# Kernel optimization log

Measured on AMD Instinct MI355X. Metric: run time of the kernel, lower is better.

## Reference

```python
import jax, jax.numpy as jnp
import numpy as np

NUM_CLASSES = 2
THRESHOLD = 0.35
NEGPOS_RATIO = 7
VARIANCES = (0.1, 0.2)
B, P, O = 64, 16800, 64  # batch, num_priors, num_objs per image


def point_form(pr):
    # cxcywh -> xyxy
    return jnp.concatenate([pr[:, :2] - pr[:, 2:] / 2, pr[:, :2] + pr[:, 2:] / 2], axis=1)


def jaccard(a, b):
    # a: [A,4] xyxy, b: [Bx,4] xyxy -> IoU [A,Bx]
    lt = jnp.maximum(a[:, None, :2], b[None, :, :2])
    rb = jnp.minimum(a[:, None, 2:], b[None, :, 2:])
    wh = jnp.clip(rb - lt, 0.0)
    inter = wh[..., 0] * wh[..., 1]
    area_a = ((a[:, 2] - a[:, 0]) * (a[:, 3] - a[:, 1]))[:, None]
    area_b = ((b[:, 2] - b[:, 0]) * (b[:, 3] - b[:, 1]))[None, :]
    return inter / (area_a + area_b - inter)


def encode(matched, priors):
    # matched xyxy [P,4], priors cxcywh [P,4]
    g_cxcy = (matched[:, :2] + matched[:, 2:]) / 2 - priors[:, :2]
    g_cxcy = g_cxcy / (VARIANCES[0] * priors[:, 2:])
    g_wh = (matched[:, 2:] - matched[:, :2]) / priors[:, 2:]
    g_wh = jnp.log(g_wh) / VARIANCES[1]
    return jnp.concatenate([g_cxcy, g_wh], axis=1)


def encode_landm(matched, priors):
    # matched [P,10] -> [P,5,2]
    m = matched.reshape(-1, 5, 2)
    g = (m - priors[:, None, :2]) / (VARIANCES[0] * priors[:, None, 2:])
    return g.reshape(-1, 10)


def match_one(truths, labels, landms, priors):
    # truths [O,4], labels [O], landms [O,10]
    overlaps = jaccard(truths, point_form(priors))  # [O,P]
    best_prior_overlap = overlaps.max(axis=1)       # per-gt best IoU
    best_prior_idx = overlaps.argmax(axis=1)
    valid_gt = best_prior_overlap >= 0.2
    best_truth_overlap = overlaps.max(axis=0)       # per-prior best IoU
    best_truth_idx = overlaps.argmax(axis=0)
    # index_fill(2) only for valid gts (best_prior_idx_filter)
    bto = best_truth_overlap.at[best_prior_idx].set(
        jnp.where(valid_gt, 2.0, best_truth_overlap[best_prior_idx]))
    # ensure every gt keeps its best prior
    bti = best_truth_idx.at[best_prior_idx].set(jnp.arange(truths.shape[0]))
    matches = truths[bti]                  # [P,4]
    conf = labels[bti]                     # [P]
    conf = jnp.where(bto < THRESHOLD, 0.0, conf)
    loc = encode(matches, priors)
    landm = encode_landm(landms[bti], priors)
    return loc, conf, landm


def smooth_l1_sum(x, mask):
    ax = jnp.abs(x)
    v = jnp.where(ax < 1.0, 0.5 * ax * ax, ax - 0.5)
    return (v * mask).sum()


def setup_inputs() -> dict:
    key = jax.random.key(0)
    k1, k2, k3, k4, k5, k6, k7, k8 = jax.random.split(key, 8)
    loc_data = jax.random.normal(k1, (B, P, 4), jnp.float32)
    conf_data = jax.random.normal(k2, (B, P, NUM_CLASSES), jnp.float32)
    landm_data = jax.random.normal(k3, (B, P, 10), jnp.float32)
    # priors: cx,cy in (0,1), w,h in (0.02,0.22)
    cxy = jax.random.uniform(k4, (P, 2), jnp.float32)
    wh = jax.random.uniform(k5, (P, 2), jnp.float32) * 0.2 + 0.02
    priors = jnp.concatenate([cxy, wh], axis=1)
    # targets: valid corner boxes + landmarks + label in {1,-1}
    xy1 = jax.random.uniform(k6, (B, O, 2), jnp.float32) * 0.6
    bwh = jax.random.uniform(k7, (B, O, 2), jnp.float32) * 0.3 + 0.05
    boxes = jnp.concatenate([xy1, xy1 + bwh], axis=-1)
    lms = jax.random.uniform(k8, (B, O, 10), jnp.float32)
    lab = jnp.where(jax.random.uniform(jax.random.fold_in(key, 9), (B, O, 1)) < 0.3, -1.0, 1.0)
    targets = jnp.concatenate([boxes, lms, lab], axis=-1)
    return {"loc_data": loc_data, "conf_data": conf_data, "landm_data": landm_data,
            "priors": priors, "targets": targets}


def reference(loc_data, conf_data, landm_data, priors, targets):
    num = loc_data.shape[0]
    num_priors = priors.shape[0]
    truths = targets[:, :, :4]
    landms = targets[:, :, 4:14]
    labels = targets[:, :, -1]
    loc_t, conf_t, landm_t = jax.vmap(match_one, in_axes=(0, 0, 0, None))(
        truths, labels, landms, priors)  # [B,P,4], [B,P], [B,P,10]

    # landmark loss over conf_t > 0
    pos1 = conf_t > 0
    num_pos_landm = pos1.astype(jnp.int32).sum(axis=1, keepdims=True)
    N1 = jnp.maximum(num_pos_landm.sum().astype(jnp.float32), 1.0)
    loss_landm = smooth_l1_sum(landm_data - landm_t, pos1[..., None].astype(landm_data.dtype))

    # localization loss over conf_t != 0 ; conf_t[pos] = 1
    pos = conf_t != 0
    conf_t01 = jnp.where(pos, 1, 0)  # int {0,1}
    loss_l = smooth_l1_sum(loc_data - loc_t, pos[..., None].astype(loc_data.dtype))

    # hard negative mining on per-prior CE loss (global-max log_sum_exp, as in source)
    batch_conf = conf_data.reshape(-1, NUM_CLASSES)
    x_max = batch_conf.max()
    lse = jnp.log(jnp.exp(batch_conf - x_max).sum(axis=1, keepdims=True)) + x_max
    gathered = jnp.take_along_axis(batch_conf, conf_t01.reshape(-1, 1), axis=1)
    loss_c = (lse - gathered).reshape(num, -1)  # [B,P]; positives NOT zeroed (as in source)
    loss_idx = jnp.argsort(-loss_c, axis=1)
    idx_rank = jnp.argsort(loss_idx, axis=1)
    num_pos = pos.astype(jnp.int32).sum(axis=1, keepdims=True)  # [B,1]
    num_neg = jnp.minimum(NEGPOS_RATIO * num_pos, num_priors - 1)
    neg = idx_rank < num_neg  # [B,P]
    neg_pos = pos | neg

    # cross-entropy (sum) over selected pos+neg priors
    logp = jax.nn.log_softmax(conf_data, axis=-1)  # [B,P,C]
    ce = -jnp.take_along_axis(logp, conf_t01[..., None], axis=-1)[..., 0]
    loss_c_final = (ce * neg_pos.astype(ce.dtype)).sum()

    N = jnp.maximum(num_pos.sum().astype(jnp.float32), 1.0)
    return (loss_l / N, loss_c_final / N, loss_landm / N1)
```

## Files before the change

kernel.cpp:

```cpp
#include <hip/hip_runtime.h>
#include <math.h>

#define BN 64
#define PN 16800
#define ON 64
#define THRESH 0.35f
#define NEGPOS 7
#define GX 66
#define NBLK (BN * GX)
#define NBP 1024
#define NBTT (BN * GX)
#define NCELL 256
#define NCB 66
#define EPSW 0.0009765625f
#define IOUF 0.3499f
#define NBINS 4096
#define MAXM 4096
#define TAILT 104

struct GAcc {
  unsigned ticket;
  float sl, slm, sc;
  int np, np1;
  unsigned pad0, pad1;
};

__device__ __forceinline__ unsigned f2key(float f) {
  unsigned u = __float_as_uint(f);
  return (u & 0x80000000u) ? ~u : (u | 0x80000000u);
}
__device__ __forceinline__ float key2f(unsigned k) {
  unsigned u = (k & 0x80000000u) ? (k & 0x7FFFFFFFu) : ~k;
  return __uint_as_float(u);
}
__device__ __forceinline__ float sl1(float d) {
  float a = fabsf(d);
  return (a < 1.f) ? 0.5f * a * a : a - 0.5f;
}

__global__ void k_count(const float* __restrict__ priors,
                        unsigned char* __restrict__ pcell,
                        unsigned* __restrict__ gcnt,
                        unsigned* __restrict__ gmax) {
  __shared__ unsigned lcnt[NCELL];
  int tid = threadIdx.x;
  lcnt[tid] = 0;
  __syncthreads();
  int p = blockIdx.x * 256 + tid;
  float mw = 0.f, mh = 0.f;
  if (p < PN) {
    float4 pr = reinterpret_cast<const float4*>(priors)[p];
    int cx = (int)(pr.x * 16.f); cx = cx < 0 ? 0 : (cx > 15 ? 15 : cx);
    int cy = (int)(pr.y * 16.f); cy = cy < 0 ? 0 : (cy > 15 ? 15 : cy);
    int cell = cy * 16 + cx;
    pcell[p] = (unsigned char)cell;
    atomicAdd(&lcnt[cell], 1u);
    mw = pr.z * 0.5f;
    mh = pr.w * 0.5f;
  }
#pragma unroll
  for (int off = 32; off; off >>= 1) {
    mw = fmaxf(mw, __shfl_xor(mw, off));
    mh = fmaxf(mh, __shfl_xor(mh, off));
  }
  if ((tid & 63) == 0) {
    atomicMax(&gmax[0], __float_as_uint(mw));
    atomicMax(&gmax[1], __float_as_uint(mh));
  }
  __syncthreads();
  unsigned c = lcnt[tid];
  if (c) atomicAdd(&gcnt[tid], c);
}

__global__ void k_scatter(const float* __restrict__ priors,
                          const float* __restrict__ targets,
                          const unsigned char* __restrict__ pcell,
                          const unsigned* __restrict__ gcnt,
                          unsigned* __restrict__ gcur,
                          const unsigned* __restrict__ gmax,
                          float4* __restrict__ sbox,
                          int* __restrict__ sorig,
                          int* __restrict__ scell,
                          int* __restrict__ inv,
                          int* __restrict__ cellOff,
                          unsigned long long* __restrict__ tmask) {
  int bid = blockIdx.x;
  int tid = threadIdx.x;
  if (bid < NCB) {
    __shared__ unsigned tmp[NCELL];
    __shared__ unsigned excl[NCELL];
    __shared__ unsigned lcnt[NCELL];
    __shared__ unsigned lbase[NCELL];
    unsigned c = gcnt[tid];
    tmp[tid] = c;
    lcnt[tid] = 0;
    __syncthreads();
    for (int off = 1; off < NCELL; off <<= 1) {
      unsigned v = (tid >= off) ? tmp[tid - off] : 0u;
      __syncthreads();
      tmp[tid] += v;
      __syncthreads();
    }
    excl[tid] = tmp[tid] - c;
    if (bid == 0) {
      cellOff[tid] = (int)(tmp[tid] - c);
      if (tid == 0) cellOff[NCELL] = PN;
    }
    __syncthreads();
    int p = bid * 256 + tid;
    bool valid = p < PN;
    int cell = 0; unsigned lrank = 0;
    if (valid) {
      cell = pcell[p];
      lrank = atomicAdd(&lcnt[cell], 1u);
    }
    __syncthreads();
    if (lcnt[tid]) lbase[tid] = atomicAdd(&gcur[tid], lcnt[tid]);
    __syncthreads();
    if (valid) {
      int slot = (int)(excl[cell] + lbase[cell] + lrank);
      float4 pr = reinterpret_cast<const float4*>(priors)[p];
      float px1 = pr.x - pr.z * 0.5f, py1 = pr.y - pr.w * 0.5f;
      float px2 = pr.x + pr.z * 0.5f, py2 = pr.y + pr.w * 0.5f;
      sbox[slot] = make_float4(px1, py1, px2, py2);
      sorig[slot] = p;
      scell[slot] = cell;
      inv[p] = slot;
    }
  } else {
    int b = bid - NCB;
    __shared__ float4 tb[ON];
    if (tid < ON) {
      const float* tg = &targets[((long)b * ON + tid) * 15];
      tb[tid] = make_float4(tg[0], tg[1], tg[2], tg[3]);
    }
    __syncthreads();
    float MW = __uint_as_float(gmax[0]), MH = __uint_as_float(gmax[1]);
    int cx = tid & 15, cy = tid >> 4;
    float cxl = (float)cx * 0.0625f, cxh = (float)(cx + 1) * 0.0625f;
    float cyl = (float)cy * 0.0625f, cyh = (float)(cy + 1) * 0.0625f;
    float pmaxa = 4.f * MW * MH;
    unsigned long long m = 0ull;
    for (int t = 0; t < ON; t++) {
      float4 a = tb[t];
      float wt = a.z - a.x, ht = a.w - a.y;
      float at = wt * ht;
      float need = IOUF * at;
      float wmin = need / fminf(ht, 2.f * MH);
      float hmin = need / fminf(wt, 2.f * MW);
      float wx0 = a.x + wmin - MW - EPSW, wx1 = a.z - wmin + MW + EPSW;
      float wy0 = a.y + hmin - MH - EPSW, wy1 = a.w - hmin + MH + EPSW;
      bool ok = (pmaxa >= need) &&
                (cxh > wx0) && (cxl < wx1) &&
                (cyh > wy0) && (cyl < wy1);
      if (ok) m |= (1ull << t);
    }
    tmask[b * NCELL + tid] = m;
  }
}

__global__ void k_pair(const float* __restrict__ targets,
                       const float4* __restrict__ sbox,
                       const int* __restrict__ sorig,
                       const int* __restrict__ scell,
                       const int* __restrict__ cellOff,
                       const unsigned* __restrict__ gmax,
                       const unsigned long long* __restrict__ tmask,
                       unsigned char* __restrict__ btpack,
                       unsigned long long* __restrict__ bpp) {
  int bid = blockIdx.x;
  int tid = threadIdx.x;

  if (bid < NBP) {
    int lane = tid & 63, wv = tid >> 6;
    int b = bid >> 4;
    int t = ((bid & 15) << 2) + wv;
    const float* tg = &targets[((long)b * ON + t) * 15];
    float ax1 = tg[0], ay1 = tg[1], ax2 = tg[2], ay2 = tg[3];
    float aa = (ax2 - ax1) * (ay2 - ay1);
    float MW = __uint_as_float(gmax[0]), MH = __uint_as_float(gmax[1]);
    int xlo = (int)floorf((ax1 - MW - EPSW) * 16.f); xlo = xlo < 0 ? 0 : (xlo > 15 ? 15 : xlo);
    int xhi = (int)floorf((ax2 + MW + EPSW) * 16.f); xhi = xhi < 0 ? 0 : (xhi > 15 ? 15 : xhi);
    int ylo = (int)floorf((ay1 - MH - EPSW) * 16.f); ylo = ylo < 0 ? 0 : (ylo > 15 ? 15 : ylo);
    int yhi = (int)floorf((ay2 + MH + EPSW) * 16.f); yhi = yhi < 0 ? 0 : (yhi > 15 ? 15 : yhi);
    float bi = 0.f, bu = 1.f; int bp = 0;
    for (int cy = ylo; cy <= yhi; cy++) {
      int s0 = cellOff[cy * 16 + xlo];
      int s1 = cellOff[cy * 16 + xhi + 1];
      for (int s = s0 + lane; s < s1; s += 64) {
        float4 pr = sbox[s];
        int op = sorig[s];
        float ab2 = (pr.z - pr.x) * (pr.w - pr.y);
        float lx = fmaxf(ax1, pr.x), ly = fmaxf(ay1, pr.y);
        float rx = fminf(ax2, pr.z), ry = fminf(ay2, pr.w);
        float w = fmaxf(rx - lx, 0.f), h = fmaxf(ry - ly, 0.f);
        float inter = w * h;
        float uni = aa + ab2 - inter;
        float A = inter * bu, C = bi * uni;
        if (A > C || (A == C && op < bp)) { bi = inter; bu = uni; bp = op; }
      }
    }
#pragma unroll
    for (int off = 1; off < 64; off <<= 1) {
      float oi = __shfl_xor(bi, off), ou = __shfl_xor(bu, off);
      int op = __shfl_xor(bp, off);
      float A = oi * bu, C = bi * ou;
      if (A > C || (A == C && op < bp)) { bi = oi; bu = ou; bp = op; }
    }
    if (lane == 0) {
      float q = bi / bu;
      bpp[(long)b * ON + t] = ((unsigned long long)f2key(q) << 32) | (unsigned)(~bp);
    }
  } else {
    int id2 = bid - NBP;
    int b = id2 / GX;
    int slab = id2 - b * GX;
    int s = slab * 256 + tid;
    bool valid = s < PN;
    int sc = valid ? s : PN - 1;
    __shared__ float4 tb[ON];
    __shared__ float ta[ON];
    if (tid < ON) {
      const float* tg = &targets[((long)b * ON + tid) * 15];
      float4 bx = make_float4(tg[0], tg[1], tg[2], tg[3]);
      tb[tid] = bx;
      ta[tid] = (bx.z - bx.x) * (bx.w - bx.y);
    }
    __syncthreads();
    float4 pr = sbox[sc];
    float ab2 = (pr.z - pr.x) * (pr.w - pr.y);
    unsigned long long um = valid ? tmask[b * NCELL + scell[sc]] : 0ull;
#pragma unroll
    for (int off = 1; off < 64; off <<= 1) um |= __shfl_xor(um, off);
    unsigned mlo = (unsigned)__builtin_amdgcn_readfirstlane((int)(unsigned)um);
    unsigned mhi = (unsigned)__builtin_amdgcn_readfirstlane((int)(unsigned)(um >> 32));
    unsigned long long m = ((unsigned long long)mhi << 32) | mlo;
    float bi = 0.f, bu = 1.f; int id = 0;
    while (m) {
      int t0 = __builtin_ctzll(m); m &= m - 1;
      float4 a0 = tb[t0]; float aa0 = ta[t0];
      if (m) {
        int t1 = __builtin_ctzll(m); m &= m - 1;
        float4 a1 = tb[t1]; float aa1 = ta[t1];
        float lx0 = fmaxf(a0.x, pr.x), ly0 = fmaxf(a0.y, pr.y);
        float rx0 = fminf(a0.z, pr.z), ry0 = fminf(a0.w, pr.w);
        float w0 = fmaxf(rx0 - lx0, 0.f), h0 = fmaxf(ry0 - ly0, 0.f);
        float in0 = w0 * h0, un0 = aa0 + ab2 - in0;
        float lx1 = fmaxf(a1.x, pr.x), ly1 = fmaxf(a1.y, pr.y);
        float rx1 = fminf(a1.z, pr.z), ry1 = fminf(a1.w, pr.w);
        float w1 = fmaxf(rx1 - lx1, 0.f), h1 = fmaxf(ry1 - ly1, 0.f);
        float in1 = w1 * h1, un1 = aa1 + ab2 - in1;
        if (in0 * bu > bi * un0) { bi = in0; bu = un0; id = t0; }
        if (in1 * bu > bi * un1) { bi = in1; bu = un1; id = t1; }
      } else {
        float lx = fmaxf(a0.x, pr.x), ly = fmaxf(a0.y, pr.y);
        float rx = fminf(a0.z, pr.z), ry = fminf(a0.w, pr.w);
        float w = fmaxf(rx - lx, 0.f), h = fmaxf(ry - ly, 0.f);
        float inter = w * h;
        float uni = aa0 + ab2 - inter;
        if (inter * bu > bi * uni) { bi = inter; bu = uni; id = t0; }
      }
    }
    if (valid) {
      float q = bi / bu;
      unsigned char posb = (q >= THRESH) ? 1 : 0;
      btpack[(long)b * PN + s] = (unsigned char)((id << 1) | posb);
    }
  }
}

__global__ void k_encode(const float* __restrict__ loc_data,
                         const float* __restrict__ conf_data,
                         const float* __restrict__ landm_data,
                         const float* __restrict__ priors,
                         const float* __restrict__ targets,
                         const unsigned char* __restrict__ btpack,
                         const int* __restrict__ inv,
                         const unsigned long long* __restrict__ bpp,
                         float* __restrict__ lossc, unsigned char* __restrict__ posf,
                         float* __restrict__ part_l, float* __restrict__ part_lm,
                         int* __restrict__ np_part, int* __restrict__ np1_part) {
  int b = blockIdx.y;
  int p = blockIdx.x * 256 + threadIdx.x;
  int bid = b * GX + blockIdx.x;
  __shared__ float4 tgs4[ON * 15 / 4];
  __shared__ int ovr[256];
  float* tgs = (float*)tgs4;
  if (threadIdx.x < ON * 15 / 4)
    tgs4[threadIdx.x] = reinterpret_cast<const float4*>(targets + (long)b * ON * 15)[threadIdx.x];
  ovr[threadIdx.x] = -1;
  __syncthreads();
  if (threadIdx.x < ON) {
    int t = threadIdx.x;
    unsigned long long best = bpp[(long)b * ON + t];
    float q = key2f((unsigned)(best >> 32));
    int qp = (int)(~(unsigned)best);
    int s0 = blockIdx.x * 256;
    if (qp >= s0 && qp < s0 + 256) {
      int valid = (q >= 0.2f) ? 1 : 0;
      atomicMax(&ovr[qp - s0], (t << 1) | valid);
    }
  }
  __syncthreads();

  float sum_l = 0.f, sum_lm = 0.f;
  int cp = 0, cp1 = 0;
  if (p < PN) {
    unsigned pk = btpack[(long)b * PN + inv[p]];
    int t = (int)(pk >> 1);
    bool pos = (pk & 1u) != 0;
    int o = ovr[threadIdx.x];
    if (o >= 0) { t = o >> 1; if (o & 1) pos = true; }
    const float* tg = &tgs[t * 15];
    float label = tg[14];
    bool pos1 = pos && (label > 0.f);
    float4 pr = reinterpret_cast<const float4*>(priors)[p];
    if (pos) {
      float rz = 1.0f / pr.z, rw = 1.0f / pr.w;
      float m0 = tg[0], m1 = tg[1], m2 = tg[2], m3 = tg[3];
      float g0 = ((m0 + m2) * 0.5f - pr.x) * rz * 10.f;
      float g1 = ((m1 + m3) * 0.5f - pr.y) * rw * 10.f;
      float g2 = __logf((m2 - m0) * rz) * 5.f;
      float g3 = __logf((m3 - m1) * rw) * 5.f;
      const float* ld = &loc_data[((long)b * PN + p) * 4];
      sum_l = sl1(ld[0] - g0) + sl1(ld[1] - g1) + sl1(ld[2] - g2) + sl1(ld[3] - g3);
      cp = 1;
      if (pos1) {
        const float* lm = &landm_data[((long)b * PN + p) * 10];
#pragma unroll
        for (int i = 0; i < 5; i++) {
          float gx = (tg[4 + 2 * i] - pr.x) * rz * 10.f;
          float gy = (tg[5 + 2 * i] - pr.y) * rw * 10.f;
          sum_lm += sl1(lm[2 * i] - gx) + sl1(lm[2 * i + 1] - gy);
        }
        cp1 = 1;
      }
    }
    float2 c2 = reinterpret_cast<const float2*>(conf_data)[(long)b * PN + p];
    float m = fmaxf(c2.x, c2.y);
    float lse = m + __logf(__expf(c2.x - m) + __expf(c2.y - m));
    lossc[b * PN + p] = lse - (pos ? c2.y : c2.x);
    posf[b * PN + p] = pos ? 1 : 0;
  }
  for (int off = 32; off; off >>= 1) {
    sum_l += __shfl_down(sum_l, off);
    sum_lm += __shfl_down(sum_lm, off);
    cp += __shfl_down(cp, off);
    cp1 += __shfl_down(cp1, off);
  }
  __shared__ float sl4[4], slm4[4];
  __shared__ int sp4[4], sp14[4];
  int w = threadIdx.x >> 6;
  if ((threadIdx.x & 63) == 0) { sl4[w] = sum_l; slm4[w] = sum_lm; sp4[w] = cp; sp14[w] = cp1; }
  __syncthreads();
  if (threadIdx.x == 0) {
    part_l[bid] = sl4[0] + sl4[1] + sl4[2] + sl4[3];
    part_lm[bid] = slm4[0] + slm4[1] + slm4[2] + slm4[3];
    np_part[bid] = sp4[0] + sp4[1] + sp4[2] + sp4[3];
    np1_part[bid] = sp14[0] + sp14[1] + sp14[2] + sp14[3];
  }
}

__global__ void __launch_bounds__(1024) k_select(const float* __restrict__ lossc,
                                                 const unsigned char* __restrict__ posf,
                                                 const int* __restrict__ np_part,
                                                 const int* __restrict__ np1_part,
                                                 const float* __restrict__ part_l,
                                                 const float* __restrict__ part_lm,
                                                 GAcc* __restrict__ gacc,
                                                 float* __restrict__ out) {
  int b = blockIdx.x;
  int tid = threadIdx.x;
  int lane = tid & 63;
  int wv = tid >> 6;
  __shared__ unsigned hist[NBINS];
  __shared__ unsigned wtot[16];
  __shared__ float resv[MAXM];
  __shared__ int residx[MAXM];
  __shared__ int s_np, s_B, s_kp;
  __shared__ unsigned s_mc;
  const float* row = &lossc[(long)b * PN];
  const unsigned char* prow = &posf[(long)b * PN];

  if (tid == 0) s_np = 0;
  for (int i = tid; i < NBINS; i += 1024) hist[i] = 0;
  __syncthreads();
  if (tid < GX) atomicAdd(&s_np, np_part[b * GX + tid]);

  const float4* rf4 = reinterpret_cast<const float4*>(row);
  const uint4* pw4 = reinterpret_cast<const uint4*>(prow);
  bool hasTail = tid < TAILT;
  float vm[16];
  float vt[4];
  {
    float4 L0 = rf4[tid * 4], L1 = rf4[tid * 4 + 1], L2 = rf4[tid * 4 + 2], L3 = rf4[tid * 4 + 3];
    vm[0] = L0.x; vm[1] = L0.y; vm[2] = L0.z; vm[3] = L0.w;
    vm[4] = L1.x; vm[5] = L1.y; vm[6] = L1.z; vm[7] = L1.w;
    vm[8] = L2.x; vm[9] = L2.y; vm[10] = L2.z; vm[11] = L2.w;
    vm[12] = L3.x; vm[13] = L3.y; vm[14] = L3.z; vm[15] = L3.w;
  }
  unsigned pmask = 0;
  {
    uint4 W = pw4[tid];
    unsigned w0 = W.x, w1 = W.y, w2 = W.z, w3 = W.w;
#pragma unroll
    for (int j = 0; j < 4; j++) {
      pmask |= ((w0 >> (8 * j)) & 1u) << j;
      pmask |= ((w1 >> (8 * j)) & 1u) << (4 + j);
      pmask |= ((w2 >> (8 * j)) & 1u) << (8 + j);
      pmask |= ((w3 >> (8 * j)) & 1u) << (12 + j);
    }
  }
  unsigned tmask = 0;
  if (hasTail) {
    float4 Lt = rf4[4096 + tid];
    vt[0] = Lt.x; vt[1] = Lt.y; vt[2] = Lt.z; vt[3] = Lt.w;
    unsigned Wt = reinterpret_cast<const unsigned*>(prow)[4096 + tid];
#pragma unroll
    for (int j = 0; j < 4; j++) tmask |= ((Wt >> (8 * j)) & 1u) << j;
  } else {
    vt[0] = vt[1] = vt[2] = vt[3] = -1.f;
  }
  int bm[16], bt4[4];
#pragma unroll
  for (int j = 0; j < 16; j++) {
    int q = (int)(vm[j] * 256.0f);
    bm[j] = q < 0 ? 0 : (q > NBINS - 1 ? NBINS - 1 : q);
  }
#pragma unroll
  for (int j = 0; j < 4; j++) {
    int q = (int)(vt[j] * 256.0f);
    bt4[j] = q < 0 ? 0 : (q > NBINS - 1 ? NBINS - 1 : q);
  }
  __syncthreads();
  int np = s_np;
  int k = NEGPOS * np;
  if (k > PN - 1) k = PN - 1;
  bool haveNeg = (k > 0);

  int B = NBINS, kp = 0, m = 0;
  bool allB = false, fallback = false;
  if (haveNeg) {
#pragma unroll
    for (int j = 0; j < 16; j++) atomicAdd(&hist[bm[j]], 1u);
    if (hasTail) {
#pragma unroll
      for (int j = 0; j < 4; j++) atomicAdd(&hist[bt4[j]], 1u);
    }
    __syncthreads();
    int t4 = tid * 4;
    unsigned h0 = hist[t4], h1 = hist[t4 + 1], h2 = hist[t4 + 2], h3 = hist[t4 + 3];
    unsigned th = h0 + h1 + h2 + h3;
    unsigned v = th;
#pragma unroll
    for (int off = 1; off < 64; off <<= 1) {
      unsigned tv = (unsigned)__shfl_down((int)v, off);
      if (lane + off < 64) v += tv;
    }
    if (lane == 0) wtot[wv] = v;
    __syncthreads();
    unsigned add = 0;
    for (int w2 = wv + 1; w2 < 16; w2++) add += wtot[w2];
    unsigned S_t = v + add;
    unsigned S_next = S_t - th;
    if (S_t >= (unsigned)k && S_next < (unsigned)k) {
      unsigned run = S_next; int Bl; unsigned kpl;
      if (run + h3 >= (unsigned)k) { Bl = t4 + 3; kpl = k - run; }
      else { run += h3;
        if (run + h2 >= (unsigned)k) { Bl = t4 + 2; kpl = k - run; }
        else { run += h2;
          if (run + h1 >= (unsigned)k) { Bl = t4 + 1; kpl = k - run; }
          else { run += h1; Bl = t4; kpl = k - run; } } }
      s_B = Bl; s_kp = (int)kpl;
    }
    __syncthreads();
    B = s_B; kp = s_kp; m = (int)hist[B];
    allB = (kp == m);
    fallback = (!allB && m > MAXM);
  }

  float acc = 0.f;
  if (haveNeg && !allB && !fallback) {
    if (tid == 0) s_mc = 0;
    __syncthreads();
#pragma unroll
    for (int j = 0; j < 16; j++) {
      if (bm[j] == B) {
        unsigned slot = atomicAdd(&s_mc, 1u);
        resv[slot] = vm[j];
        residx[slot] = (tid * 16 + j) | (((pmask >> j) & 1u) ? 0x40000000 : 0);
      }
    }
    if (hasTail) {
#pragma unroll
      for (int j = 0; j < 4; j++) {
        if (bt4[j] == B) {
          unsigned slot = atomicAdd(&s_mc, 1u);
          resv[slot] = vt[j];
          residx[slot] = (16384 + tid * 4 + j) | (((tmask >> j) & 1u) ? 0x40000000 : 0);
        }
      }
    }
    __syncthreads();
    for (int i = tid; i < m; i += 1024) {
      float vi = resv[i];
      int pk = residx[i];
      int ii = pk & 0x3FFFFFFF;
      bool posi = (pk & 0x40000000) != 0;
      int rank = 0;
      for (int j = 0; j < m; j++) {
        float vj = resv[j];
        int ij = residx[j] & 0x3FFFFFFF;
        rank += (vj > vi || (vj == vi && ij < ii)) ? 1 : 0;
      }
      if (rank < kp && !posi) acc += vi;
    }
  }

  unsigned T = 0, R = 0, C = 0;
  if (fallback) {
    __shared__ unsigned s_lo, s_hi, fcnt[16];
    if (tid == 0) { s_lo = 0u; s_hi = 0xFFFFFFFFu; }
    __syncthreads();
    for (int it = 0; it < 32; it++) {
      unsigned lo = s_lo, hi = s_hi;
      unsigned mid = lo + ((hi - lo) >> 1) + ((hi - lo) & 1u);
      unsigned c = 0;
#pragma unroll
      for (int j = 0; j < 16; j++) c += (f2key(vm[j]) >= mid) ? 1u : 0u;
      if (hasTail) {
#pragma unroll
        for (int j = 0; j < 4; j++) c += (f2key(vt[j]) >= mid) ? 1u : 0u;
      }
#pragma unroll
      for (int o = 32; o; o >>= 1) c += (unsigned)__shfl_down((int)c, o);
      if (lane == 0) fcnt[wv] = c;
      __syncthreads();
      if (tid == 0) {
        unsigned tot = 0;
        for (int i = 0; i < 16; i++) tot += fcnt[i];
        if (tot >= (unsigned)k) s_lo = mid; else s_hi = mid - 1;
      }
      __syncthreads();
      if (s_lo >= s_hi) break;
    }
    T = s_lo;
    unsigned cg = 0, ce = 0;
#pragma unroll
    for (int j = 0; j < 16; j++) {
      unsigned key = f2key(vm[j]);
      cg += (key > T) ? 1u : 0u;
      ce += (key == T) ? 1u : 0u;
    }
    if (hasTail) {
#pragma unroll
      for (int j = 0; j < 4; j++) {
        unsigned key = f2key(vt[j]);
        cg += (key > T) ? 1u : 0u;
        ce += (key == T) ? 1u : 0u;
      }
    }
#pragma unroll
    for (int o = 32; o; o >>= 1) {
      cg += (unsigned)__shfl_down((int)cg, o);
      ce += (unsigned)__shfl_down((int)ce, o);
    }
    if (lane == 0) { fcnt[wv] = cg; wtot[wv] = ce; }
    __syncthreads();
    if (tid == 0) {
      unsigned tg2 = 0, te = 0;
      for (int i = 0; i < 16; i++) { tg2 += fcnt[i]; te += wtot[i]; }
      fcnt[0] = tg2; wtot[0] = te;
    }
    __syncthreads();
    C = wtot[0];
    R = (unsigned)k - fcnt[0];
    if (C != R && tid < 64) {
      unsigned running = 0;
      for (int base2 = 0; base2 < PN; base2 += 64) {
        int p = base2 + tid;
        bool tie = false, pos = false;
        float v2 = 0.f;
        if (p < PN) { v2 = row[p]; tie = (f2key(v2) == T); pos = prow[p] != 0; }
        unsigned long long mm = __ballot(tie);
        if (tie) {
          unsigned rank = running + (unsigned)__popcll(mm & ((1ull << tid) - 1));
          if (rank < R && !pos) acc += v2;
        }
        running += (unsigned)__popcll(mm);
      }
    }
  }

  unsigned ptc = 0;
#pragma unroll
  for (int j = 0; j < 16; j++) {
    float v2 = vm[j];
    bool pos = (pmask >> j) & 1u;
    if (pos) acc += v2;
    else if (haveNeg) {
      if (!fallback) {
        if (bm[j] > B || (bm[j] == B && allB)) acc += v2;
      } else {
        if (f2key(v2) > T) acc += v2;
      }
    }
    if (fallback && pos && f2key(v2) == T) ptc++;
  }
  if (hasTail) {
#pragma unroll
    for (int j = 0; j < 4; j++) {
      float v2 = vt[j];
      bool pos = (tmask >> j) & 1u;
      if (pos) acc += v2;
      else if (haveNeg) {
        if (!fallback) {
          if (bt4[j] > B || (bt4[j] == B && allB)) acc += v2;
        } else {
          if (f2key(v2) > T) acc += v2;
        }
      }
      if (fallback && pos && f2key(v2) == T) ptc++;
    }
  }
  for (int o = 32; o; o >>= 1) {
    acc += __shfl_down(acc, o);
    ptc += __shfl_down(ptc, o);
  }
  __shared__ float wsum[16];
  __shared__ unsigned wpt[16];
  if (lane == 0) { wsum[wv] = acc; wpt[wv] = ptc; }
  __syncthreads();

  __shared__ float s_rsl, s_rslm;
  __shared__ int s_rnp1;
  if (tid == 0) { s_rsl = 0.f; s_rslm = 0.f; s_rnp1 = 0; }
  __syncthreads();
  if (tid < GX) {
    atomicAdd(&s_rsl, part_l[b * GX + tid]);
    atomicAdd(&s_rslm, part_lm[b * GX + tid]);
    atomicAdd(&s_rnp1, np1_part[b * GX + tid]);
  }
  __syncthreads();

  if (tid == 0) {
    float tot = 0.f; unsigned pt = 0;
    for (int i = 0; i < 16; i++) { tot += wsum[i]; pt += wpt[i]; }
    if (fallback && C == R) tot += (float)(C - pt) * key2f(T);
    atomicAdd(&gacc->sc, tot);
    atomicAdd(&gacc->sl, s_rsl);
    atomicAdd(&gacc->slm, s_rslm);
    atomicAdd(&gacc->np, np);
    atomicAdd(&gacc->np1, s_rnp1);
  }
  __threadfence();
  __shared__ int lastF;
  if (tid == 0) lastF = (atomicAdd(&gacc->ticket, 1u) == (unsigned)(BN - 1)) ? 1 : 0;
  __syncthreads();
  if (lastF && tid == 0) {
    __threadfence();
    float sl = atomicAdd(&gacc->sl, 0.f);
    float slm = atomicAdd(&gacc->slm, 0.f);
    float sc = atomicAdd(&gacc->sc, 0.f);
    int tnp = atomicAdd(&gacc->np, 0);
    int tnp1 = atomicAdd(&gacc->np1, 0);
    float N = fmaxf((float)tnp, 1.f);
    float N1 = fmaxf((float)tnp1, 1.f);
    out[0] = sl / N;
    out[1] = sc / N;
    out[2] = slm / N1;
  }
}

extern "C" void kernel_launch(void* const* d_in, const int* in_sizes, int n_in,
                              void* d_out, int out_size, void* d_ws, size_t ws_size,
                              hipStream_t stream) {
  const float* loc_data = (const float*)d_in[0];
  const float* conf_data = (const float*)d_in[1];
  const float* landm_data = (const float*)d_in[2];
  const float* priors = (const float*)d_in[3];
  const float* targets = (const float*)d_in[4];
  float* out = (float*)d_out;

  char* ws = (char*)d_ws;
  size_t off = 0;
  float* lossc = (float*)(ws + off); off += (size_t)BN * PN * 4;
  unsigned char* btpack = (unsigned char*)(ws + off); off += (size_t)BN * PN;
  unsigned char* posf = (unsigned char*)(ws + off); off += (size_t)BN * PN;
  off = (off + 15) & ~(size_t)15;
  unsigned long long* bpp = (unsigned long long*)(ws + off); off += (size_t)BN * ON * 8;
  float* part_l = (float*)(ws + off); off += NBLK * 4;
  float* part_lm = (float*)(ws + off); off += NBLK * 4;
  int* np_part = (int*)(ws + off); off += NBLK * 4;
  int* np1_part = (int*)(ws + off); off += NBLK * 4;
  float4* sbox = (float4*)(ws + off); off += (size_t)PN * 16;
  int* sorig = (int*)(ws + off); off += (size_t)PN * 4;
  int* scell = (int*)(ws + off); off += (size_t)PN * 4;
  int* inv = (int*)(ws + off); off += (size_t)PN * 4;
  unsigned char* pcell = (unsigned char*)(ws + off); off += (size_t)PN;
  off = (off + 15) & ~(size_t)15;
  int* cellOff = (int*)(ws + off); off += 260 * 4;
  unsigned long long* tmask = (unsigned long long*)(ws + off); off += (size_t)BN * NCELL * 8;
  off = (off + 15) & ~(size_t)15;
  unsigned* zreg = (unsigned*)(ws + off);
  unsigned* gcnt = zreg;
  unsigned* gcur = zreg + 256;
  unsigned* gmax = zreg + 512;
  GAcc* gacc = (GAcc*)(zreg + 516);
  size_t zbytes = (256 + 256 + 4) * 4 + sizeof(GAcc);
  off += zbytes;

  hipMemsetAsync(zreg, 0, zbytes, stream);
  k_count<<<NCB, 256, 0, stream>>>(priors, pcell, gcnt, gmax);
  k_scatter<<<NCB + BN, 256, 0, stream>>>(priors, targets, pcell, gcnt, gcur, gmax,
                                          sbox, sorig, scell, inv, cellOff, tmask);
  k_pair<<<NBP + NBTT, 256, 0, stream>>>(targets, sbox, sorig, scell, cellOff, gmax,
                                         tmask, btpack, bpp);
  dim3 gbp(GX, BN);
  k_encode<<<gbp, 256, 0, stream>>>(loc_data, conf_data, landm_data, priors, targets,
                                    btpack, inv, bpp, lossc, posf,
                                    part_l, part_lm, np_part, np1_part);
  k_select<<<BN, 1024, 0, stream>>>(lossc, posf, np_part, np1_part, part_l, part_lm,
                                    gacc, out);
}
```

Before: 197.4 us.

## Fuse per-prior best-truth IoU search into encode kernel, drop btpack/inv buffers

The per-prior best-truth search no longer runs in k_pair, which wrote a packed byte array in sorted order and needed an inverse permutation. k_encode now does that search itself, in the original prior order. It loads the cell masks and GT boxes into shared memory and loops over the candidate truths for each prior's cell. This removes a B*P byte write and read, the inv/scell arrays, and half of the k_pair grid. In exchange the mask is per-thread rather than wave-uniform, so lanes diverge in the while loop, and k_encode uses more shared memory.

Result: slower. 206.7 us (+4.7%).

```diff
diff --git a/kernel.cpp b/kernel.cpp
--- a/kernel.cpp
+++ b/kernel.cpp
@@ -9,7 +9,6 @@
 #define GX 66
 #define NBLK (BN * GX)
 #define NBP 1024
-#define NBTT (BN * GX)
 #define NCELL 256
 #define NCB 66
 #define EPSW 0.0009765625f
@@ -80,8 +79,6 @@
                           const unsigned* __restrict__ gmax,
                           float4* __restrict__ sbox,
                           int* __restrict__ sorig,
-                          int* __restrict__ scell,
-                          int* __restrict__ inv,
                           int* __restrict__ cellOff,
                           unsigned long long* __restrict__ tmask) {
   int bid = blockIdx.x;
@@ -124,8 +121,6 @@
       float px2 = pr.x + pr.z * 0.5f, py2 = pr.y + pr.w * 0.5f;
       sbox[slot] = make_float4(px1, py1, px2, py2);
       sorig[slot] = p;
-      scell[slot] = cell;
-      inv[p] = slot;
     }
   } else {
     int b = bid - NCB;
@@ -159,113 +154,52 @@
   }
 }
 
-__global__ void k_pair(const float* __restrict__ targets,
-                       const float4* __restrict__ sbox,
-                       const int* __restrict__ sorig,
-                       const int* __restrict__ scell,
-                       const int* __restrict__ cellOff,
-                       const unsigned* __restrict__ gmax,
-                       const unsigned long long* __restrict__ tmask,
-                       unsigned char* __restrict__ btpack,
-                       unsigned long long* __restrict__ bpp) {
+__global__ void k_bp(const float* __restrict__ targets,
+                     const float4* __restrict__ sbox,
+                     const int* __restrict__ sorig,
+                     const int* __restrict__ cellOff,
+                     const unsigned* __restrict__ gmax,
+                     unsigned long long* __restrict__ bpp) {
   int bid = blockIdx.x;
   int tid = threadIdx.x;
-
-  if (bid < NBP) {
-    int lane = tid & 63, wv = tid >> 6;
-    int b = bid >> 4;
-    int t = ((bid & 15) << 2) + wv;
-    const float* tg = &targets[((long)b * ON + t) * 15];
-    float ax1 = tg[0], ay1 = tg[1], ax2 = tg[2], ay2 = tg[3];
-    float aa = (ax2 - ax1) * (ay2 - ay1);
-    float MW = __uint_as_float(gmax[0]), MH = __uint_as_float(gmax[1]);
-    int xlo = (int)floorf((ax1 - MW - EPSW) * 16.f); xlo = xlo < 0 ? 0 : (xlo > 15 ? 15 : xlo);
-    int xhi = (int)floorf((ax2 + MW + EPSW) * 16.f); xhi = xhi < 0 ? 0 : (xhi > 15 ? 15 : xhi);
-    int ylo = (int)floorf((ay1 - MH - EPSW) * 16.f); ylo = ylo < 0 ? 0 : (ylo > 15 ? 15 : ylo);
-    int yhi = (int)floorf((ay2 + MH + EPSW) * 16.f); yhi = yhi < 0 ? 0 : (yhi > 15 ? 15 : yhi);
-    float bi = 0.f, bu = 1.f; int bp = 0;
-    for (int cy = ylo; cy <= yhi; cy++) {
-      int s0 = cellOff[cy * 16 + xlo];
-      int s1 = cellOff[cy * 16 + xhi + 1];
-      for (int s = s0 + lane; s < s1; s += 64) {
-        float4 pr = sbox[s];
-        int op = sorig[s];
-        float ab2 = (pr.z - pr.x) * (pr.w - pr.y);
-        float lx = fmaxf(ax1, pr.x), ly = fmaxf(ay1, pr.y);
-        float rx = fminf(ax2, pr.z), ry = fminf(ay2, pr.w);
-        float w = fmaxf(rx - lx, 0.f), h = fmaxf(ry - ly, 0.f);
-        float inter = w * h;
-        float uni = aa + ab2 - inter;
-        float A = inter * bu, C = bi * uni;
-        if (A > C || (A == C && op < bp)) { bi = inter; bu = uni; bp = op; }
-      }
-    }
-#pragma unroll
-    for (int off = 1; off < 64; off <<= 1) {
-      float oi = __shfl_xor(bi, off), ou = __shfl_xor(bu, off);
-      int op = __shfl_xor(bp, off);
-      float A = oi * bu, C = bi * ou;
-      if (A > C || (A == C && op < bp)) { bi = oi; bu = ou; bp = op; }
-    }
-    if (lane == 0) {
-      float q = bi / bu;
-      bpp[(long)b * ON + t] = ((unsigned long long)f2key(q) << 32) | (unsigned)(~bp);
-    }
-  } else {
-    int id2 = bid - NBP;
-    int b = id2 / GX;
-    int slab = id2 - b * GX;
-    int s = slab * 256 + tid;
-    bool valid = s < PN;
-    int sc = valid ? s : PN - 1;
-    __shared__ float4 tb[ON];
-    __shared__ float ta[ON];
-    if (tid < ON) {
-      const float* tg = &targets[((long)b * ON + tid) * 15];
-      float4 bx = make_float4(tg[0], tg[1], tg[2], tg[3]);
-      tb[tid] = bx;
-      ta[tid] = (bx.z - bx.x) * (bx.w - bx.y);
-    }
-    __syncthreads();
-    float4 pr = sbox[sc];
-    float ab2 = (pr.z - pr.x) * (pr.w - pr.y);
-    unsigned long long um = valid ? tmask[b * NCELL + scell[sc]] : 0ull;
-#pragma unroll
-    for (int off = 1; off < 64; off <<= 1) um |= __shfl_xor(um, off);
-    unsigned mlo = (unsigned)__builtin_amdgcn_readfirstlane((int)(unsigned)um);
-    unsigned mhi = (unsigned)__builtin_amdgcn_readfirstlane((int)(unsigned)(um >> 32));
-    unsigned long long m = ((unsigned long long)mhi << 32) | mlo;
-    float bi = 0.f, bu = 1.f; int id = 0;
-    while (m) {
-      int t0 = __builtin_ctzll(m); m &= m - 1;
-      float4 a0 = tb[t0]; float aa0 = ta[t0];
-      if (m) {
-        int t1 = __builtin_ctzll(m); m &= m - 1;
-        float4 a1 = tb[t1]; float aa1 = ta[t1];
-        float lx0 = fmaxf(a0.x, pr.x), ly0 = fmaxf(a0.y, pr.y);
-        float rx0 = fminf(a0.z, pr.z), ry0 = fminf(a0.w, pr.w);
-        float w0 = fmaxf(rx0 - lx0, 0.f), h0 = fmaxf(ry0 - ly0, 0.f);
-        float in0 = w0 * h0, un0 = aa0 + ab2 - in0;
-        float lx1 = fmaxf(a1.x, pr.x), ly1 = fmaxf(a1.y, pr.y);
-        float rx1 = fminf(a1.z, pr.z), ry1 = fminf(a1.w, pr.w);
-        float w1 = fmaxf(rx1 - lx1, 0.f), h1 = fmaxf(ry1 - ly1, 0.f);
-        float in1 = w1 * h1, un1 = aa1 + ab2 - in1;
-        if (in0 * bu > bi * un0) { bi = in0; bu = un0; id = t0; }
-        if (in1 * bu > bi * un1) { bi = in1; bu = un1; id = t1; }
-      } else {
-        float lx = fmaxf(a0.x, pr.x), ly = fmaxf(a0.y, pr.y);
-        float rx = fminf(a0.z, pr.z), ry = fminf(a0.w, pr.w);
-        float w = fmaxf(rx - lx, 0.f), h = fmaxf(ry - ly, 0.f);
-        float inter = w * h;
-        float uni = aa0 + ab2 - inter;
-        if (inter * bu > bi * uni) { bi = inter; bu = uni; id = t0; }
-      }
-    }
-    if (valid) {
-      float q = bi / bu;
-      unsigned char posb = (q >= THRESH) ? 1 : 0;
-      btpack[(long)b * PN + s] = (unsigned char)((id << 1) | posb);
-    }
+  int lane = tid & 63, wv = tid >> 6;
+  int b = bid >> 4;
+  int t = ((bid & 15) << 2) + wv;
+  const float* tg = &targets[((long)b * ON + t) * 15];
+  float ax1 = tg[0], ay1 = tg[1], ax2 = tg[2], ay2 = tg[3];
+  float aa = (ax2 - ax1) * (ay2 - ay1);
+  float MW = __uint_as_float(gmax[0]), MH = __uint_as_float(gmax[1]);
+  int xlo = (int)floorf((ax1 - MW - EPSW) * 16.f); xlo = xlo < 0 ? 0 : (xlo > 15 ? 15 : xlo);
+  int xhi = (int)floorf((ax2 + MW + EPSW) * 16.f); xhi = xhi < 0 ? 0 : (xhi > 15 ? 15 : xhi);
+  int ylo = (int)floorf((ay1 - MH - EPSW) * 16.f); ylo = ylo < 0 ? 0 : (ylo > 15 ? 15 : ylo);
+  int yhi = (int)floorf((ay2 + MH + EPSW) * 16.f); yhi = yhi < 0 ? 0 : (yhi > 15 ? 15 : yhi);
+  float bi = 0.f, bu = 1.f; int bp = 0;
+  for (int cy = ylo; cy <= yhi; cy++) {
+    int s0 = cellOff[cy * 16 + xlo];
+    int s1 = cellOff[cy * 16 + xhi + 1];
+    for (int s = s0 + lane; s < s1; s += 64) {
+      float4 pr = sbox[s];
+      int op = sorig[s];
+      float ab2 = (pr.z - pr.x) * (pr.w - pr.y);
+      float lx = fmaxf(ax1, pr.x), ly = fmaxf(ay1, pr.y);
+      float rx = fminf(ax2, pr.z), ry = fminf(ay2, pr.w);
+      float w = fmaxf(rx - lx, 0.f), h = fmaxf(ry - ly, 0.f);
+      float inter = w * h;
+      float uni = aa + ab2 - inter;
+      float A = inter * bu, C = bi * uni;
+      if (A > C || (A == C && op < bp)) { bi = inter; bu = uni; bp = op; }
+    }
+  }
+#pragma unroll
+  for (int off = 1; off < 64; off <<= 1) {
+    float oi = __shfl_xor(bi, off), ou = __shfl_xor(bu, off);
+    int op = __shfl_xor(bp, off);
+    float A = oi * bu, C = bi * ou;
+    if (A > C || (A == C && op < bp)) { bi = oi; bu = ou; bp = op; }
+  }
+  if (lane == 0) {
+    float q = bi / bu;
+    bpp[(long)b * ON + t] = ((unsigned long long)f2key(q) << 32) | (unsigned)(~bp);
   }
 }
 
@@ -274,8 +208,8 @@
                          const float* __restrict__ landm_data,
                          const float* __restrict__ priors,
                          const float* __restrict__ targets,
-                         const unsigned char* __restrict__ btpack,
-                         const int* __restrict__ inv,
+                         const unsigned char* __restrict__ pcell,
+                         const unsigned long long* __restrict__ tmask,
                          const unsigned long long* __restrict__ bpp,
                          float* __restrict__ lossc, unsigned char* __restrict__ posf,
                          float* __restrict__ part_l, float* __restrict__ part_lm,
@@ -284,10 +218,20 @@
   int p = blockIdx.x * 256 + threadIdx.x;
   int bid = b * GX + blockIdx.x;
   __shared__ float4 tgs4[ON * 15 / 4];
+  __shared__ float4 tb[ON];
+  __shared__ float ta[ON];
+  __shared__ unsigned long long smask[NCELL];
   __shared__ int ovr[256];
   float* tgs = (float*)tgs4;
   if (threadIdx.x < ON * 15 / 4)
     tgs4[threadIdx.x] = reinterpret_cast<const float4*>(targets + (long)b * ON * 15)[threadIdx.x];
+  smask[threadIdx.x] = tmask[b * NCELL + threadIdx.x];
+  if (threadIdx.x < ON) {
+    const float* tg = &targets[((long)b * ON + threadIdx.x) * 15];
+    float4 bx = make_float4(tg[0], tg[1], tg[2], tg[3]);
+    tb[threadIdx.x] = bx;
+    ta[threadIdx.x] = (bx.z - bx.x) * (bx.w - bx.y);
+  }
   ovr[threadIdx.x] = -1;
   __syncthreads();
   if (threadIdx.x < ON) {
@@ -306,15 +250,28 @@
   float sum_l = 0.f, sum_lm = 0.f;
   int cp = 0, cp1 = 0;
   if (p < PN) {
-    unsigned pk = btpack[(long)b * PN + inv[p]];
-    int t = (int)(pk >> 1);
-    bool pos = (pk & 1u) != 0;
+    float4 pr = reinterpret_cast<const float4*>(priors)[p];
+    float px1 = pr.x - pr.z * 0.5f, py1 = pr.y - pr.w * 0.5f;
+    float px2 = pr.x + pr.z * 0.5f, py2 = pr.y + pr.w * 0.5f;
+    float ab2 = (px2 - px1) * (py2 - py1);
+    unsigned long long m = smask[pcell[p]];
+    float bi = 0.f, bu = 1.f; int t = 0;
+    while (m) {
+      int t0 = __builtin_ctzll(m); m &= m - 1;
+      float4 a0 = tb[t0];
+      float lx = fmaxf(a0.x, px1), ly = fmaxf(a0.y, py1);
+      float rx = fminf(a0.z, px2), ry = fminf(a0.w, py2);
+      float w2 = fmaxf(rx - lx, 0.f), h2 = fmaxf(ry - ly, 0.f);
+      float inter = w2 * h2;
+      float uni = ta[t0] + ab2 - inter;
+      if (inter * bu > bi * uni) { bi = inter; bu = uni; t = t0; }
+    }
+    bool pos = (bi / bu) >= THRESH;
     int o = ovr[threadIdx.x];
     if (o >= 0) { t = o >> 1; if (o & 1) pos = true; }
     const float* tg = &tgs[t * 15];
     float label = tg[14];
     bool pos1 = pos && (label > 0.f);
-    float4 pr = reinterpret_cast<const float4*>(priors)[p];
     if (pos) {
       float rz = 1.0f / pr.z, rw = 1.0f / pr.w;
       float m0 = tg[0], m1 = tg[1], m2 = tg[2], m3 = tg[3];
@@ -337,8 +294,8 @@
       }
     }
     float2 c2 = reinterpret_cast<const float2*>(conf_data)[(long)b * PN + p];
-    float m = fmaxf(c2.x, c2.y);
-    float lse = m + __logf(__expf(c2.x - m) + __expf(c2.y - m));
+    float mx = fmaxf(c2.x, c2.y);
+    float lse = mx + __logf(__expf(c2.x - mx) + __expf(c2.y - mx));
     lossc[b * PN + p] = lse - (pos ? c2.y : c2.x);
     posf[b * PN + p] = pos ? 1 : 0;
   }
@@ -685,7 +642,6 @@
   char* ws = (char*)d_ws;
   size_t off = 0;
   float* lossc = (float*)(ws + off); off += (size_t)BN * PN * 4;
-  unsigned char* btpack = (unsigned char*)(ws + off); off += (size_t)BN * PN;
   unsigned char* posf = (unsigned char*)(ws + off); off += (size_t)BN * PN;
   off = (off + 15) & ~(size_t)15;
   unsigned long long* bpp = (unsigned long long*)(ws + off); off += (size_t)BN * ON * 8;
@@ -695,8 +651,6 @@
   int* np1_part = (int*)(ws + off); off += NBLK * 4;
   float4* sbox = (float4*)(ws + off); off += (size_t)PN * 16;
   int* sorig = (int*)(ws + off); off += (size_t)PN * 4;
-  int* scell = (int*)(ws + off); off += (size_t)PN * 4;
-  int* inv = (int*)(ws + off); off += (size_t)PN * 4;
   unsigned char* pcell = (unsigned char*)(ws + off); off += (size_t)PN;
   off = (off + 15) & ~(size_t)15;
   int* cellOff = (int*)(ws + off); off += 260 * 4;
@@ -713,12 +667,11 @@
   hipMemsetAsync(zreg, 0, zbytes, stream);
   k_count<<<NCB, 256, 0, stream>>>(priors, pcell, gcnt, gmax);
   k_scatter<<<NCB + BN, 256, 0, stream>>>(priors, targets, pcell, gcnt, gcur, gmax,
-                                          sbox, sorig, scell, inv, cellOff, tmask);
-  k_pair<<<NBP + NBTT, 256, 0, stream>>>(targets, sbox, sorig, scell, cellOff, gmax,
-                                         tmask, btpack, bpp);
+                                          sbox, sorig, cellOff, tmask);
+  k_bp<<<NBP, 256, 0, stream>>>(targets, sbox, sorig, cellOff, gmax, bpp);
   dim3 gbp(GX, BN);
   k_encode<<<gbp, 256, 0, stream>>>(loc_data, conf_data, landm_data, priors, targets,
-                                    btpack, inv, bpp, lossc, posf,
+                                    pcell, tmask, bpp, lossc, posf,
                                     part_l, part_lm, np_part, np1_part);
   k_select<<<BN, 1024, 0, stream>>>(lossc, posf, np_part, np1_part, part_l, part_lm,
                                     gacc, out);
```
